# Performance work log

Measured on AMD Instinct MI355X. Metric: run time of the kernel, lower is better.

Reference implementation:

```python
import jax, jax.numpy as jnp
import numpy as np

EMBED = 512
EXPAND = 1024


def setup_inputs() -> dict:
    key = jax.random.key(0)
    k1, k2, k3, k4, k5 = jax.random.split(key, 5)
    B, C, P, N = 4, EMBED, 16, 1024
    x = jax.random.normal(k1, (B, C, P, N), dtype=jnp.float32)
    # 1x1 conv weights == per-pixel linear maps over the channel dim
    Wqkv = jax.random.normal(k2, (1 + 2 * EXPAND, C), dtype=jnp.float32) * (1.0 / np.sqrt(C))
    bqkv = jax.random.normal(k3, (1 + 2 * EXPAND,), dtype=jnp.float32) * 0.01
    Wout = jax.random.normal(k4, (C, EXPAND), dtype=jnp.float32) * (1.0 / np.sqrt(EXPAND))
    bout = jax.random.normal(k5, (C,), dtype=jnp.float32) * 0.01
    return {"x": x, "Wqkv": Wqkv, "bqkv": bqkv, "Wout": Wout, "bout": bout}


def reference(x, Wqkv, bqkv, Wout, bout):
    # qkv 1x1 conv: (B,C,P,N) -> (B, 1+2E, P, N)
    qkv = jnp.einsum('oc,bcpn->bopn', Wqkv, x) + bqkv[None, :, None, None]
    E = EXPAND
    query = qkv[:, :1]            # (B,1,P,N)
    key_t = qkv[:, 1:1 + E]       # (B,E,P,N)
    value = qkv[:, 1 + E:]        # (B,E,P,N)
    # softmax over patches dim (last axis); attn_dropout p=0.0 -> identity
    context_scores = jax.nn.softmax(query, axis=-1)
    # weighted sum over N, keepdim -> (B,E,P,1)
    context_vector = jnp.sum(key_t * context_scores, axis=-1, keepdims=True)
    # broadcast gate
    out = jax.nn.relu(value) * context_vector  # (B,E,P,N)
    # out 1x1 conv back to embed channels
    out = jnp.einsum('oe,bepn->bopn', Wout, out) + bout[None, :, None, None]
    return out
```

## Files before the change

### kernel.cpp

```cpp
#include <hip/hip_runtime.h>

#define EMBED 512
#define EXPAND 1024
#define PNUM 16
#define NLEN 1024
#define CHW (PNUM * NLEN)
#define SLABS 64

typedef unsigned short u16;
typedef unsigned int u32;
typedef __bf16 bf16x8 __attribute__((ext_vector_type(8)));
typedef u16 u16x8 __attribute__((ext_vector_type(8)));
typedef float f32x4 __attribute__((ext_vector_type(4)));

__device__ __forceinline__ u16 f2bf(float f) {
  u32 u = __builtin_bit_cast(u32, f);
  return (u16)((u + 0x7FFFu + ((u >> 16) & 1u)) >> 16);
}
__device__ __forceinline__ float bf2f(u16 h) {
  return __builtin_bit_cast(float, (u32)h << 16);
}
__device__ __forceinline__ void gld16(const u16* g, u16* l) {
  __builtin_amdgcn_global_load_lds((__attribute__((address_space(1))) void*)g,
                                   (__attribute__((address_space(3))) void*)l,
                                   16, 0, 0);
}
__device__ __forceinline__ f32x4 MFMA(bf16x8 a, bf16x8 b, f32x4 c) {
  return __builtin_amdgcn_mfma_f32_16x16x32_bf16(a, b, c, 0, 0, 0);
}

__global__ __launch_bounds__(256) void k_convert_w(
    const float* __restrict__ Wqkv, const float* __restrict__ Wout,
    u16* __restrict__ WvB, u16* __restrict__ WoutB) {
  const int NV = EXPAND * EMBED;
  int idx = (blockIdx.x * 256 + threadIdx.x) * 4;
  if (idx < NV) {
    float4 v = *(const float4*)(Wqkv + (size_t)(1 + EXPAND) * EMBED + idx);
    uint2 u = make_uint2((u32)f2bf(v.x) | ((u32)f2bf(v.y) << 16),
                         (u32)f2bf(v.z) | ((u32)f2bf(v.w) << 16));
    *(uint2*)(WvB + idx) = u;
  } else {
    int j = idx - NV;
    float4 v = *(const float4*)(Wout + j);
    uint2 u = make_uint2((u32)f2bf(v.x) | ((u32)f2bf(v.y) << 16),
                         (u32)f2bf(v.z) | ((u32)f2bf(v.w) << 16));
    *(uint2*)(WoutB + j) = u;
  }
}

__global__ __launch_bounds__(256) void k_convert_x(
    const float* __restrict__ x, const float* __restrict__ Wqkv,
    float* __restrict__ qpart, u16* __restrict__ xbT) {
  __shared__ __align__(16) u16 tile[128 * 64];
  __shared__ float qp[256 * 4];
  const int slab = blockIdx.x >> 4;
  const int nw = (blockIdx.x >> 1) & 7;
  const int chalf = blockIdx.x & 1;
  const int b = slab >> 4, p = slab & 15;
  const int t = threadIdx.x;
  const int c8 = t & 7;
  const int ng = t >> 3;
  const float* xs = x + (size_t)b * (EMBED * CHW) + (size_t)p * NLEN + nw * 128;
  u16* dst = xbT + (size_t)slab * (NLEN * EMBED) + (size_t)(nw * 128) * EMBED;
  float qa[4] = {0.f, 0.f, 0.f, 0.f};

  for (int cc = 0; cc < 4; ++cc) {
    const int cbase = chalf * 256 + cc * 64;
    float4 v[8];
#pragma unroll
    for (int k = 0; k < 8; ++k)
      v[k] = *(const float4*)(xs + (size_t)(cbase + c8 * 8 + k) * CHW + ng * 4);
    const float* w0 = Wqkv + cbase + c8 * 8;
#pragma unroll
    for (int k = 0; k < 8; ++k) {
      qa[0] += w0[k] * v[k].x;
      qa[1] += w0[k] * v[k].y;
      qa[2] += w0[k] * v[k].z;
      qa[3] += w0[k] * v[k].w;
    }
#pragma unroll
    for (int j = 0; j < 4; ++j) {
      const int nl = ng * 4 + j;
      float e[8];
#pragma unroll
      for (int k = 0; k < 8; ++k)
        e[k] = (j == 0) ? v[k].x : (j == 1) ? v[k].y : (j == 2) ? v[k].z : v[k].w;
      uint4 pk;
      pk.x = (u32)f2bf(e[0]) | ((u32)f2bf(e[1]) << 16);
      pk.y = (u32)f2bf(e[2]) | ((u32)f2bf(e[3]) << 16);
      pk.z = (u32)f2bf(e[4]) | ((u32)f2bf(e[5]) << 16);
      pk.w = (u32)f2bf(e[6]) | ((u32)f2bf(e[7]) << 16);
      *(uint4*)(tile + nl * 64 + ((c8 ^ (nl & 7)) << 3)) = pk;
    }
    __syncthreads();
#pragma unroll
    for (int m = 0; m < 4; ++m) {
      const int s = m * 256 + t;
      const int nl = s >> 3, ch = s & 7;
      uint4 vv = *(const uint4*)(tile + nl * 64 + ((ch ^ (nl & 7)) << 3));
      *(uint4*)(dst + (size_t)nl * EMBED + cbase + ch * 8) = vv;
    }
    __syncthreads();
  }
  qp[t * 4 + 0] = qa[0];
  qp[t * 4 + 1] = qa[1];
  qp[t * 4 + 2] = qa[2];
  qp[t * 4 + 3] = qa[3];
  __syncthreads();
  if (t < 128) {
    float a = 0.f;
#pragma unroll
    for (int o = 0; o < 8; ++o) a += qp[((((t >> 2) << 3) + o) << 2) + (t & 3)];
    qpart[(size_t)slab * 2048 + chalf * 1024 + nw * 128 + t] = a;
  }
}

__global__ __launch_bounds__(256) void k_attn1(
    const float* __restrict__ qpart, const u16* __restrict__ xbT,
    float* __restrict__ ypart) {
  __shared__ float red[4];
  __shared__ float sm[128];
  __shared__ float yp[4][512];
  const int slab = blockIdx.x >> 3, n8 = blockIdx.x & 7;
  const int t = threadIdx.x, w = t >> 6, l = t & 63;
  const float* q0 = qpart + (size_t)slab * 2048;
  const float* q1 = q0 + 1024;

  float4 qa = ((const float4*)q0)[t];
  float4 qb = ((const float4*)q1)[t];
  float4 q4 = make_float4(qa.x + qb.x, qa.y + qb.y, qa.z + qb.z, qa.w + qb.w);
  float m = fmaxf(fmaxf(q4.x, q4.y), fmaxf(q4.z, q4.w));
#pragma unroll
  for (int sh = 32; sh; sh >>= 1) m = fmaxf(m, __shfl_xor(m, sh, 64));
  if (l == 0) red[w] = m;
  __syncthreads();
  float gm = fmaxf(fmaxf(red[0], red[1]), fmaxf(red[2], red[3]));
  float s = __expf(q4.x - gm) + __expf(q4.y - gm) + __expf(q4.z - gm) + __expf(q4.w - gm);
#pragma unroll
  for (int sh = 32; sh; sh >>= 1) s += __shfl_xor(s, sh, 64);
  __syncthreads();
  if (l == 0) red[w] = s;
  __syncthreads();
  float gs = red[0] + red[1] + red[2] + red[3];
  if (t < 128) {
    const int n = n8 * 128 + t;
    sm[t] = __expf(q0[n] + q1[n] - gm) / gs;
  }
  __syncthreads();

  float ya[8] = {0.f, 0.f, 0.f, 0.f, 0.f, 0.f, 0.f, 0.f};
  const u16* xs = xbT + (size_t)slab * (NLEN * EMBED) + (size_t)(n8 * 128) * EMBED;
  for (int ni = 0; ni < 32; ++ni) {
    const int nloc = ni * 4 + w;
    const float sc = sm[nloc];
    u16x8 v = *(const u16x8*)(xs + (size_t)nloc * EMBED + l * 8);
#pragma unroll
    for (int j = 0; j < 8; ++j) ya[j] += sc * bf2f(v[j]);
  }
#pragma unroll
  for (int j = 0; j < 8; ++j) yp[w][l * 8 + j] = ya[j];
  __syncthreads();
  for (int c = t; c < 512; c += 256)
    ypart[((size_t)slab * 8 + n8) * 512 + c] = yp[0][c] + yp[1][c] + yp[2][c] + yp[3][c];
}

__global__ __launch_bounds__(256) void k_attn2(
    const float* __restrict__ ypart, const float* __restrict__ Wqkv,
    const float* __restrict__ bqkv, float* __restrict__ cv) {
  __shared__ float yl[512];
  const int slab = blockIdx.x >> 2, ec = blockIdx.x & 3;
  const int t = threadIdx.x;
  const int e = ec * 256 + t;
  const float* yb = ypart + (size_t)slab * 8 * 512;
  for (int c = t; c < 512; c += 256) {
    float a = 0.f;
#pragma unroll
    for (int k = 0; k < 8; ++k) a += yb[k * 512 + c];
    yl[c] = a;
  }
  __syncthreads();
  const float* wk = Wqkv + (size_t)(1 + e) * EMBED;
  float a = 0.f;
#pragma unroll 4
  for (int c0 = 0; c0 < EMBED; c0 += 4) {
    float4 wv = *(const float4*)(wk + c0);
    a += wv.x * yl[c0] + wv.y * yl[c0 + 1] + wv.z * yl[c0 + 2] + wv.w * yl[c0 + 3];
  }
  cv[(size_t)slab * EXPAND + e] = a + bqkv[1 + e];
}

template <int K, int NT>
__device__ __forceinline__ void gemm256(const u16* __restrict__ Abase,
                                        const u16* __restrict__ Bbase,
                                        u16* lds, f32x4 (&acc)[8][4]) {
  const int t = threadIdx.x;
  const int w = t >> 6, l = t & 63;
  const int wr = w >> 2, wc = w & 3;
  const int lr = l & 15, lj = l >> 4;

  int oa[8][2], ob[4][2];
#pragma unroll
  for (int mi = 0; mi < 8; ++mi)
#pragma unroll
    for (int kc = 0; kc < 2; ++kc) {
      const int row = wr * 128 + mi * 16 + lr;
      oa[mi][kc] = row * 64 + (((kc * 4 + lj) ^ (row & 7)) << 3);
    }
#pragma unroll
  for (int ni = 0; ni < 4; ++ni)
#pragma unroll
    for (int kc = 0; kc < 2; ++kc) {
      const int row = wc * 64 + ni * 16 + lr;
      ob[ni][kc] = row * 64 + (((kc * 4 + lj) ^ (row & 7)) << 3);
    }
  int gofs[4], dofs[4];
#pragma unroll
  for (int i = 0; i < 4; ++i) {
    const int s = i * 512 + t;
    const int row = s >> 3, pch = s & 7;
    gofs[i] = row * K + ((pch ^ (row & 7)) << 3);
    dofs[i] = s * 8;
  }
  auto st1 = [&](u16* dstBase, const u16* gBase, int kt, int i) {
    gld16(gBase + gofs[i] + kt, dstBase + dofs[i]);
  };

  u16* bA0 = lds;
  u16* bB0 = lds + 16384;
  u16* bA1 = lds + 32768;
  u16* bB1 = lds + 49152;

  st1(bA0, Abase, 0, 0); st1(bA0, Abase, 0, 1);
  st1(bA0, Abase, 0, 2); st1(bA0, Abase, 0, 3);
  st1(bB0, Bbase, 0, 0); st1(bB0, Bbase, 0, 1);
  st1(bB0, Bbase, 0, 2); st1(bB0, Bbase, 0, 3);
  st1(bA1, Abase, 64, 0); st1(bA1, Abase, 64, 1);
  st1(bA1, Abase, 64, 2); st1(bA1, Abase, 64, 3);
  st1(bB1, Bbase, 64, 0); st1(bB1, Bbase, 64, 1);
  st1(bB1, Bbase, 64, 2); st1(bB1, Bbase, 64, 3);
  asm volatile("s_waitcnt vmcnt(8)" ::: "memory");
  __builtin_amdgcn_s_barrier();

#pragma unroll 1
  for (int kt = 0; kt < NT; ++kt) {
    u16* bufA = lds + (kt & 1) * 32768;
    u16* bufB = bufA + 16384;
    const bool st2 = (kt + 2) < NT;
    const int k2 = (kt + 2) * 64;
    bf16x8 a0[4][2], a1[4][2], b0[2][2], b1[2][2];

#pragma unroll
    for (int mi = 0; mi < 4; ++mi)
#pragma unroll
      for (int kc = 0; kc < 2; ++kc)
        a0[mi][kc] = *(const bf16x8*)(bufA + oa[mi][kc]);
#pragma unroll
    for (int ni = 0; ni < 2; ++ni)
#pragma unroll
      for (int kc = 0; kc < 2; ++kc)
        b0[ni][kc] = *(const bf16x8*)(bufB + ob[ni][kc]);
    __builtin_amdgcn_s_barrier();
    __builtin_amdgcn_s_setprio(1);
#pragma unroll
    for (int mi = 0; mi < 4; ++mi)
#pragma unroll
      for (int ni = 0; ni < 2; ++ni)
#pragma unroll
        for (int kc = 0; kc < 2; ++kc)
          acc[mi][ni] = MFMA(a0[mi][kc], b0[ni][kc], acc[mi][ni]);
    __builtin_amdgcn_s_setprio(0);
    __builtin_amdgcn_s_barrier();

#pragma unroll
    for (int ni = 0; ni < 2; ++ni)
#pragma unroll
      for (int kc = 0; kc < 2; ++kc)
        b1[ni][kc] = *(const bf16x8*)(bufB + ob[ni + 2][kc]);
    if (st2) {
      st1(bufA, Abase, k2, 0); st1(bufA, Abase, k2, 2);
      st1(bufB, Bbase, k2, 0); st1(bufB, Bbase, k2, 1);
    }
    __builtin_amdgcn_s_barrier();
    __builtin_amdgcn_s_setprio(1);
#pragma unroll
    for (int mi = 0; mi < 4; ++mi)
#pragma unroll
      for (int ni = 0; ni < 2; ++ni)
#pragma unroll
        for (int kc = 0; kc < 2; ++kc)
          acc[mi][ni + 2] = MFMA(a0[mi][kc], b1[ni][kc], acc[mi][ni + 2]);
    __builtin_amdgcn_s_setprio(0);
    __builtin_amdgcn_s_barrier();

#pragma unroll
    for (int mi = 0; mi < 4; ++mi)
#pragma unroll
      for (int kc = 0; kc < 2; ++kc)
        a1[mi][kc] = *(const bf16x8*)(bufA + oa[mi + 4][kc]);
    if (st2) { st1(bufB, Bbase, k2, 2); st1(bufB, Bbase, k2, 3); }
    __builtin_amdgcn_s_barrier();
    __builtin_amdgcn_s_setprio(1);
#pragma unroll
    for (int mi = 0; mi < 4; ++mi)
#pragma unroll
      for (int ni = 0; ni < 2; ++ni)
#pragma unroll
        for (int kc = 0; kc < 2; ++kc)
          acc[mi + 4][ni + 2] = MFMA(a1[mi][kc], b1[ni][kc], acc[mi + 4][ni + 2]);
    __builtin_amdgcn_s_setprio(0);
    __builtin_amdgcn_s_barrier();

    if (st2) { st1(bufA, Abase, k2, 1); st1(bufA, Abase, k2, 3); }
    __builtin_amdgcn_s_barrier();
    __builtin_amdgcn_s_setprio(1);
#pragma unroll
    for (int mi = 0; mi < 4; ++mi)
#pragma unroll
      for (int ni = 0; ni < 2; ++ni)
#pragma unroll
        for (int kc = 0; kc < 2; ++kc)
          acc[mi + 4][ni] = MFMA(a1[mi][kc], b0[ni][kc], acc[mi + 4][ni]);
    __builtin_amdgcn_s_setprio(0);
    if (st2)
      asm volatile("s_waitcnt vmcnt(8)" ::: "memory");
    else
      asm volatile("s_waitcnt vmcnt(0)" ::: "memory");
    __builtin_amdgcn_s_barrier();
  }
}

__global__ __launch_bounds__(512, 2) void k_gemm1(
    const u16* __restrict__ xbT, const u16* __restrict__ WvB,
    const float* __restrict__ bqkv, const float* __restrict__ cv,
    u16* __restrict__ midT) {
  __shared__ __align__(16) u16 lds[65536];
  const int bid = blockIdx.x;
  const int xc = bid & 7, k = bid >> 3;
  const int te = k & 3;
  const int gg = ((k >> 2) << 3) | xc;
  const int slab = gg >> 2, tn = gg & 3;
  const u16* A = xbT + (size_t)slab * (NLEN * EMBED) + (size_t)tn * 256 * EMBED;
  const u16* B = WvB + (size_t)te * 256 * EMBED;
  f32x4 acc[8][4];
  const f32x4 z = {0.f, 0.f, 0.f, 0.f};
#pragma unroll
  for (int i = 0; i < 8; ++i)
#pragma unroll
    for (int j = 0; j < 4; ++j) acc[i][j] = z;
  gemm256<EMBED, 8>(A, B, lds, acc);

  const int t = threadIdx.x, w = t >> 6, l = t & 63;
  const int wr = w >> 2, wc = w & 3;
  const int lr = l & 15, lq4 = (l >> 4) * 4;
#pragma unroll
  for (int ni = 0; ni < 4; ++ni) {
    const int col = wc * 64 + ni * 16 + lr;
    const int e = te * 256 + col;
    const float bv = bqkv[1 + EXPAND + e];
    const float cve = cv[(size_t)slab * EXPAND + e];
#pragma unroll
    for (int mi = 0; mi < 8; ++mi) {
      const int nr = wr * 128 + mi * 16 + lq4;
#pragma unroll
      for (int r = 0; r < 4; ++r) {
        float v = acc[mi][ni][r] + bv;
        v = v > 0.f ? v * cve : 0.f;
        const int row = nr + r;
        lds[row * 256 + ((((col >> 3) ^ (row & 7)) << 3) | (col & 7))] = f2bf(v);
      }
    }
  }
  __syncthreads();
  u16* mt = midT + (size_t)slab * (NLEN * EXPAND) + (size_t)te * 256;
#pragma unroll
  for (int it = 0; it < 16; ++it) {
    const int row = w * 32 + it * 2 + (l >> 5);
    const int ch = (l & 31) ^ (row & 7);
    uint4 v = *(const uint4*)(lds + row * 256 + ch * 8);
    *(uint4*)(mt + (size_t)(tn * 256 + row) * EXPAND + (l & 31) * 8) = v;
  }
}

__global__ __launch_bounds__(512, 2) void k_gemm2(
    const u16* __restrict__ midT, const u16* __restrict__ WoutB,
    const float* __restrict__ bout, float* __restrict__ out) {
  __shared__ __align__(16) u16 lds[65536];
  const int bid = blockIdx.x;
  const int xc = bid & 7, k = bid >> 3;
  const int to = k & 1;
  const int gg = ((k >> 1) << 3) | xc;
  const int slab = gg >> 2, tn = gg & 3;
  const int b = slab >> 4, p = slab & 15;
  const u16* A = midT + (size_t)slab * (NLEN * EXPAND) + (size_t)tn * 256 * EXPAND;
  const u16* B = WoutB + (size_t)to * 256 * EXPAND;
  f32x4 acc[8][4];
  const f32x4 z = {0.f, 0.f, 0.f, 0.f};
#pragma unroll
  for (int i = 0; i < 8; ++i)
#pragma unroll
    for (int j = 0; j < 4; ++j) acc[i][j] = z;
  gemm256<EXPAND, 16>(A, B, lds, acc);

  const int t = threadIdx.x, w = t >> 6, l = t & 63;
  const int wr = w >> 2, wc = w & 3;
  const int lr = l & 15, lq4 = (l >> 4) * 4;
  float* ob = out + (size_t)b * (EMBED * CHW) + (size_t)p * NLEN;
#pragma unroll
  for (int ni = 0; ni < 4; ++ni) {
    const int o = to * 256 + wc * 64 + ni * 16 + lr;
    const float bo = bout[o];
#pragma unroll
    for (int mi = 0; mi < 8; ++mi) {
      const int nr = tn * 256 + wr * 128 + mi * 16 + lq4;
      float4 v;
      v.x = acc[mi][ni][0] + bo;
      v.y = acc[mi][ni][1] + bo;
      v.z = acc[mi][ni][2] + bo;
      v.w = acc[mi][ni][3] + bo;
      *(float4*)(ob + (size_t)o * CHW + nr) = v;
    }
  }
}

extern "C" void kernel_launch(void* const* d_in, const int* in_sizes, int n_in,
                              void* d_out, int out_size, void* d_ws, size_t ws_size,
                              hipStream_t stream) {
  const float* x = (const float*)d_in[0];
  const float* Wqkv = (const float*)d_in[1];
  const float* bqkv = (const float*)d_in[2];
  const float* Wout = (const float*)d_in[3];
  const float* bout = (const float*)d_in[4];
  float* out = (float*)d_out;

  char* ws = (char*)d_ws;
  u16* xbT = (u16*)ws;
  u16* WvB = (u16*)(ws + 67108864);
  u16* WoutB = (u16*)(ws + 68157440);
  float* cv = (float*)(ws + 69468160);
  u16* midT = (u16*)(ws + 69730304);
  float* ypart = (float*)(ws + 69730304);
  float* qpart = (float*)(ws + 69730304 + 1048576);

  k_convert_w<<<1024, 256, 0, stream>>>(Wqkv, Wout, WvB, WoutB);
  k_convert_x<<<1024, 256, 0, stream>>>(x, Wqkv, qpart, xbT);
  k_attn1<<<512, 256, 0, stream>>>(qpart, xbT, ypart);
  k_attn2<<<256, 256, 0, stream>>>(ypart, Wqkv, bqkv, cv);
  k_gemm1<<<1024, 512, 0, stream>>>(xbT, WvB, bqkv, cv, midT);
  k_gemm2<<<512, 512, 0, stream>>>(midT, WoutB, bout, out);
}
```

Before: 272.3 us.

## Replace pipelined 256x256 GEMM tiles with simple single-buffered 128x128 tiles

Both projection GEMMs move from 256x256 tiles on 512 threads, with a double-buffered and interleaved prefetch/MFMA schedule, to 128x128 tiles on 256 threads with a plain load-sync-compute-sync loop. The grids grow fourfold and LDS per block drops, which allows more resident blocks per CU. In exchange each byte loaded is reused less, and global-to-LDS loads no longer overlap with MFMA work inside a block, so latency hiding depends on occupancy across blocks.

```diff
diff --git a/kernel.cpp b/kernel.cpp
--- a/kernel.cpp
+++ b/kernel.cpp
@@ -190,228 +190,137 @@
 }
 
 template <int K, int NT>
-__device__ __forceinline__ void gemm256(const u16* __restrict__ Abase,
+__device__ __forceinline__ void gemm128(const u16* __restrict__ Abase,
                                         const u16* __restrict__ Bbase,
-                                        u16* lds, f32x4 (&acc)[8][4]) {
+                                        u16* lds, f32x4 (&acc)[4][4]) {
   const int t = threadIdx.x;
   const int w = t >> 6, l = t & 63;
-  const int wr = w >> 2, wc = w & 3;
+  const int wr = w >> 1, wc = w & 1;
   const int lr = l & 15, lj = l >> 4;
-
-  int oa[8][2], ob[4][2];
-#pragma unroll
-  for (int mi = 0; mi < 8; ++mi)
-#pragma unroll
-    for (int kc = 0; kc < 2; ++kc) {
-      const int row = wr * 128 + mi * 16 + lr;
-      oa[mi][kc] = row * 64 + (((kc * 4 + lj) ^ (row & 7)) << 3);
-    }
-#pragma unroll
-  for (int ni = 0; ni < 4; ++ni)
-#pragma unroll
-    for (int kc = 0; kc < 2; ++kc) {
-      const int row = wc * 64 + ni * 16 + lr;
-      ob[ni][kc] = row * 64 + (((kc * 4 + lj) ^ (row & 7)) << 3);
-    }
-  int gofs[4], dofs[4];
-#pragma unroll
-  for (int i = 0; i < 4; ++i) {
-    const int s = i * 512 + t;
-    const int row = s >> 3, pch = s & 7;
-    gofs[i] = row * K + ((pch ^ (row & 7)) << 3);
-    dofs[i] = s * 8;
-  }
-  auto st1 = [&](u16* dstBase, const u16* gBase, int kt, int i) {
-    gld16(gBase + gofs[i] + kt, dstBase + dofs[i]);
-  };
-
-  u16* bA0 = lds;
-  u16* bB0 = lds + 16384;
-  u16* bA1 = lds + 32768;
-  u16* bB1 = lds + 49152;
-
-  st1(bA0, Abase, 0, 0); st1(bA0, Abase, 0, 1);
-  st1(bA0, Abase, 0, 2); st1(bA0, Abase, 0, 3);
-  st1(bB0, Bbase, 0, 0); st1(bB0, Bbase, 0, 1);
-  st1(bB0, Bbase, 0, 2); st1(bB0, Bbase, 0, 3);
-  st1(bA1, Abase, 64, 0); st1(bA1, Abase, 64, 1);
-  st1(bA1, Abase, 64, 2); st1(bA1, Abase, 64, 3);
-  st1(bB1, Bbase, 64, 0); st1(bB1, Bbase, 64, 1);
-  st1(bB1, Bbase, 64, 2); st1(bB1, Bbase, 64, 3);
-  asm volatile("s_waitcnt vmcnt(8)" ::: "memory");
-  __builtin_amdgcn_s_barrier();
 
 #pragma unroll 1
   for (int kt = 0; kt < NT; ++kt) {
-    u16* bufA = lds + (kt & 1) * 32768;
-    u16* bufB = bufA + 16384;
-    const bool st2 = (kt + 2) < NT;
-    const int k2 = (kt + 2) * 64;
-    bf16x8 a0[4][2], a1[4][2], b0[2][2], b1[2][2];
-
+    const int kc0 = kt * 64;
+#pragma unroll
+    for (int i = 0; i < 4; ++i) {
+      const int s = i * 256 + t;
+      const int row = s >> 3, pch = s & 7;
+      const int gch = (pch ^ (row & 7)) << 3;
+      gld16(Abase + (size_t)row * K + kc0 + gch, lds + s * 8);
+      gld16(Bbase + (size_t)row * K + kc0 + gch, lds + 8192 + s * 8);
+    }
+    __syncthreads();
+    bf16x8 af[4][2], bg[4][2];
 #pragma unroll
     for (int mi = 0; mi < 4; ++mi)
 #pragma unroll
-      for (int kc = 0; kc < 2; ++kc)
-        a0[mi][kc] = *(const bf16x8*)(bufA + oa[mi][kc]);
-#pragma unroll
-    for (int ni = 0; ni < 2; ++ni)
-#pragma unroll
-      for (int kc = 0; kc < 2; ++kc)
-        b0[ni][kc] = *(const bf16x8*)(bufB + ob[ni][kc]);
-    __builtin_amdgcn_s_barrier();
-    __builtin_amdgcn_s_setprio(1);
+      for (int kc = 0; kc < 2; ++kc) {
+        const int row = wr * 64 + mi * 16 + lr;
+        af[mi][kc] = *(const bf16x8*)(lds + row * 64 +
+                                      (((kc * 4 + lj) ^ (row & 7)) << 3));
+      }
+#pragma unroll
+    for (int ni = 0; ni < 4; ++ni)
+#pragma unroll
+      for (int kc = 0; kc < 2; ++kc) {
+        const int row = wc * 64 + ni * 16 + lr;
+        bg[ni][kc] = *(const bf16x8*)(lds + 8192 + row * 64 +
+                                      (((kc * 4 + lj) ^ (row & 7)) << 3));
+      }
 #pragma unroll
     for (int mi = 0; mi < 4; ++mi)
 #pragma unroll
-      for (int ni = 0; ni < 2; ++ni)
+      for (int ni = 0; ni < 4; ++ni)
 #pragma unroll
         for (int kc = 0; kc < 2; ++kc)
-          acc[mi][ni] = MFMA(a0[mi][kc], b0[ni][kc], acc[mi][ni]);
-    __builtin_amdgcn_s_setprio(0);
-    __builtin_amdgcn_s_barrier();
-
-#pragma unroll
-    for (int ni = 0; ni < 2; ++ni)
-#pragma unroll
-      for (int kc = 0; kc < 2; ++kc)
-        b1[ni][kc] = *(const bf16x8*)(bufB + ob[ni + 2][kc]);
-    if (st2) {
-      st1(bufA, Abase, k2, 0); st1(bufA, Abase, k2, 2);
-      st1(bufB, Bbase, k2, 0); st1(bufB, Bbase, k2, 1);
-    }
-    __builtin_amdgcn_s_barrier();
-    __builtin_amdgcn_s_setprio(1);
-#pragma unroll
-    for (int mi = 0; mi < 4; ++mi)
-#pragma unroll
-      for (int ni = 0; ni < 2; ++ni)
-#pragma unroll
-        for (int kc = 0; kc < 2; ++kc)
-          acc[mi][ni + 2] = MFMA(a0[mi][kc], b1[ni][kc], acc[mi][ni + 2]);
-    __builtin_amdgcn_s_setprio(0);
-    __builtin_amdgcn_s_barrier();
-
-#pragma unroll
-    for (int mi = 0; mi < 4; ++mi)
-#pragma unroll
-      for (int kc = 0; kc < 2; ++kc)
-        a1[mi][kc] = *(const bf16x8*)(bufA + oa[mi + 4][kc]);
-    if (st2) { st1(bufB, Bbase, k2, 2); st1(bufB, Bbase, k2, 3); }
-    __builtin_amdgcn_s_barrier();
-    __builtin_amdgcn_s_setprio(1);
-#pragma unroll
-    for (int mi = 0; mi < 4; ++mi)
-#pragma unroll
-      for (int ni = 0; ni < 2; ++ni)
-#pragma unroll
-        for (int kc = 0; kc < 2; ++kc)
-          acc[mi + 4][ni + 2] = MFMA(a1[mi][kc], b1[ni][kc], acc[mi + 4][ni + 2]);
-    __builtin_amdgcn_s_setprio(0);
-    __builtin_amdgcn_s_barrier();
-
-    if (st2) { st1(bufA, Abase, k2, 1); st1(bufA, Abase, k2, 3); }
-    __builtin_amdgcn_s_barrier();
-    __builtin_amdgcn_s_setprio(1);
-#pragma unroll
-    for (int mi = 0; mi < 4; ++mi)
-#pragma unroll
-      for (int ni = 0; ni < 2; ++ni)
-#pragma unroll
-        for (int kc = 0; kc < 2; ++kc)
-          acc[mi + 4][ni] = MFMA(a1[mi][kc], b0[ni][kc], acc[mi + 4][ni]);
-    __builtin_amdgcn_s_setprio(0);
-    if (st2)
-      asm volatile("s_waitcnt vmcnt(8)" ::: "memory");
-    else
-      asm volatile("s_waitcnt vmcnt(0)" ::: "memory");
-    __builtin_amdgcn_s_barrier();
-  }
-}
-
-__global__ __launch_bounds__(512, 2) void k_gemm1(
+          acc[mi][ni] = MFMA(af[mi][kc], bg[ni][kc], acc[mi][ni]);
+    __syncthreads();
+  }
+}
+
+__global__ __launch_bounds__(256, 3) void k_gemm1(
     const u16* __restrict__ xbT, const u16* __restrict__ WvB,
     const float* __restrict__ bqkv, const float* __restrict__ cv,
     u16* __restrict__ midT) {
-  __shared__ __align__(16) u16 lds[65536];
+  __shared__ __align__(16) u16 lds[16384];
   const int bid = blockIdx.x;
   const int xc = bid & 7, k = bid >> 3;
-  const int te = k & 3;
-  const int gg = ((k >> 2) << 3) | xc;
-  const int slab = gg >> 2, tn = gg & 3;
-  const u16* A = xbT + (size_t)slab * (NLEN * EMBED) + (size_t)tn * 256 * EMBED;
-  const u16* B = WvB + (size_t)te * 256 * EMBED;
-  f32x4 acc[8][4];
+  const int te = k & 7;
+  const int gg = ((k >> 3) << 3) | xc;
+  const int slab = gg >> 3, tn = gg & 7;
+  const u16* A = xbT + (size_t)slab * (NLEN * EMBED) + (size_t)tn * 128 * EMBED;
+  const u16* B = WvB + (size_t)te * 128 * EMBED;
+  f32x4 acc[4][4];
   const f32x4 z = {0.f, 0.f, 0.f, 0.f};
 #pragma unroll
-  for (int i = 0; i < 8; ++i)
+  for (int i = 0; i < 4; ++i)
 #pragma unroll
     for (int j = 0; j < 4; ++j) acc[i][j] = z;
-  gemm256<EMBED, 8>(A, B, lds, acc);
+  gemm128<EMBED, 8>(A, B, lds, acc);
 
   const int t = threadIdx.x, w = t >> 6, l = t & 63;
-  const int wr = w >> 2, wc = w & 3;
+  const int wr = w >> 1, wc = w & 1;
   const int lr = l & 15, lq4 = (l >> 4) * 4;
 #pragma unroll
   for (int ni = 0; ni < 4; ++ni) {
     const int col = wc * 64 + ni * 16 + lr;
-    const int e = te * 256 + col;
+    const int e = te * 128 + col;
     const float bv = bqkv[1 + EXPAND + e];
     const float cve = cv[(size_t)slab * EXPAND + e];
 #pragma unroll
-    for (int mi = 0; mi < 8; ++mi) {
-      const int nr = wr * 128 + mi * 16 + lq4;
+    for (int mi = 0; mi < 4; ++mi) {
+      const int nr = wr * 64 + mi * 16 + lq4;
 #pragma unroll
       for (int r = 0; r < 4; ++r) {
         float v = acc[mi][ni][r] + bv;
         v = v > 0.f ? v * cve : 0.f;
         const int row = nr + r;
-        lds[row * 256 + ((((col >> 3) ^ (row & 7)) << 3) | (col & 7))] = f2bf(v);
+        lds[row * 128 + ((((col >> 3) ^ (row & 7)) << 3) | (col & 7))] = f2bf(v);
       }
     }
   }
   __syncthreads();
-  u16* mt = midT + (size_t)slab * (NLEN * EXPAND) + (size_t)te * 256;
-#pragma unroll
-  for (int it = 0; it < 16; ++it) {
-    const int row = w * 32 + it * 2 + (l >> 5);
-    const int ch = (l & 31) ^ (row & 7);
-    uint4 v = *(const uint4*)(lds + row * 256 + ch * 8);
-    *(uint4*)(mt + (size_t)(tn * 256 + row) * EXPAND + (l & 31) * 8) = v;
-  }
-}
-
-__global__ __launch_bounds__(512, 2) void k_gemm2(
+  u16* mt = midT + (size_t)slab * (NLEN * EXPAND) + (size_t)te * 128;
+#pragma unroll
+  for (int it = 0; it < 8; ++it) {
+    const int row = w * 32 + it * 4 + (l >> 4);
+    const int ch = (l & 15) ^ (row & 7);
+    uint4 v = *(const uint4*)(lds + row * 128 + ch * 8);
+    *(uint4*)(mt + (size_t)(tn * 128 + row) * EXPAND + (l & 15) * 8) = v;
+  }
+}
+
+__global__ __launch_bounds__(256, 3) void k_gemm2(
     const u16* __restrict__ midT, const u16* __restrict__ WoutB,
     const float* __restrict__ bout, float* __restrict__ out) {
-  __shared__ __align__(16) u16 lds[65536];
+  __shared__ __align__(16) u16 lds[16384];
   const int bid = blockIdx.x;
   const int xc = bid & 7, k = bid >> 3;
-  const int to = k & 1;
-  const int gg = ((k >> 1) << 3) | xc;
-  const int slab = gg >> 2, tn = gg & 3;
+  const int to = k & 3;
+  const int gg = ((k >> 2) << 3) | xc;
+  const int slab = gg >> 3, tn = gg & 7;
   const int b = slab >> 4, p = slab & 15;
-  const u16* A = midT + (size_t)slab * (NLEN * EXPAND) + (size_t)tn * 256 * EXPAND;
-  const u16* B = WoutB + (size_t)to * 256 * EXPAND;
-  f32x4 acc[8][4];
+  const u16* A = midT + (size_t)slab * (NLEN * EXPAND) + (size_t)tn * 128 * EXPAND;
+  const u16* B = WoutB + (size_t)to * 128 * EXPAND;
+  f32x4 acc[4][4];
   const f32x4 z = {0.f, 0.f, 0.f, 0.f};
 #pragma unroll
-  for (int i = 0; i < 8; ++i)
+  for (int i = 0; i < 4; ++i)
 #pragma unroll
     for (int j = 0; j < 4; ++j) acc[i][j] = z;
-  gemm256<EXPAND, 16>(A, B, lds, acc);
+  gemm128<EXPAND, 16>(A, B, lds, acc);
 
   const int t = threadIdx.x, w = t >> 6, l = t & 63;
-  const int wr = w >> 2, wc = w & 3;
+  const int wr = w >> 1, wc = w & 1;
   const int lr = l & 15, lq4 = (l >> 4) * 4;
   float* ob = out + (size_t)b * (EMBED * CHW) + (size_t)p * NLEN;
 #pragma unroll
   for (int ni = 0; ni < 4; ++ni) {
-    const int o = to * 256 + wc * 64 + ni * 16 + lr;
+    const int o = to * 128 + wc * 64 + ni * 16 + lr;
     const float bo = bout[o];
 #pragma unroll
-    for (int mi = 0; mi < 8; ++mi) {
-      const int nr = tn * 256 + wr * 128 + mi * 16 + lq4;
+    for (int mi = 0; mi < 4; ++mi) {
+      const int nr = tn * 128 + wr * 64 + mi * 16 + lq4;
       float4 v;
       v.x = acc[mi][ni][0] + bo;
       v.y = acc[mi][ni][1] + bo;
@@ -445,6 +354,6 @@
   k_convert_x<<<1024, 256, 0, stream>>>(x, Wqkv, qpart, xbT);
   k_attn1<<<512, 256, 0, stream>>>(qpart, xbT, ypart);
   k_attn2<<<256, 256, 0, stream>>>(ypart, Wqkv, bqkv, cv);
-  k_gemm1<<<1024, 512, 0, stream>>>(xbT, WvB, bqkv, cv, midT);
-  k_gemm2<<<512, 512, 0, stream>>>(midT, WoutB, bout, out);
-}
+  k_gemm1<<<4096, 256, 0, stream>>>(xbT, WvB, bqkv, cv, midT);
+  k_gemm2<<<2048, 256, 0, stream>>>(midT, WoutB, bout, out);
+}
```

New measurement: 261.2 us. -4.1%, faster.
